# Kernel optimization log

Measured on AMD Instinct MI355X. Metric: run time of the kernel, lower is better.

Reference implementation:

```python
import jax, jax.numpy as jnp
import numpy as np
from jax import lax

MODES = 16
DEPTH = 8
NPH = 8  # photons = sum(init_state); init_state = [1]*8 + [0]*8
IDX = np.arange(NPH)  # output_indices derived from init_state
PI = np.pi
CHUNK = 4096  # pairs per permanent chunk (memory control, mirrors chunk_subsets idea)


def setup_inputs() -> dict:
    key = jax.random.key(0)
    k1, k2, k3 = jax.random.split(key, 3)
    x = jax.random.normal(k1, (256, 64), dtype=jnp.float32)
    W = jax.random.normal(k2, (120, 64), dtype=jnp.float32) / np.sqrt(64.0)
    b = jax.random.normal(k3, (120,), dtype=jnp.float32) * 0.01
    return {"x": x, "W": W, "b": b}


def _forward(x, W, b):
    N = x.shape[0]
    # fc1 + sigmoid embedding -> angle pairs
    x_emb = jax.nn.sigmoid(x @ W.T + b)              # (N, 120)
    tbu = x_emb.reshape(N, -1, 2)                    # (N, T, 2)
    theta = tbu[:, :, 0] * (PI / 2)
    phi = tbu[:, :, 1] * (2 * PI)
    ct = jnp.cos(theta).astype(jnp.complex64)
    st = jnp.sin(theta).astype(jnp.complex64)
    ep = jnp.exp(1j * phi.astype(jnp.complex64))
    # 2x2 tunable beam-splitter unitaries: [[e^{i phi} c, -s], [e^{i phi} s, c]]
    row0 = jnp.stack([ep * ct, -st], axis=-1)
    row1 = jnp.stack([ep * st, ct], axis=-1)
    blocks = jnp.stack([row0, row1], axis=-2)        # (N, T, 2, 2)

    # Apply block-diagonal layers. Block-diag matmul only mixes row pairs,
    # so update row segments directly instead of building (modes,modes) UBS.
    U = jnp.broadcast_to(jnp.eye(MODES, dtype=jnp.complex64), (N, MODES, MODES))
    nb_even, nb_odd = MODES // 2, (MODES - 2) // 2
    n_before = 0
    for d in range(DEPTH):
        if d % 2 == 0:
            nb, off = nb_even, 0
        else:
            nb, off = nb_odd, 1
        blk = blocks[:, n_before:n_before + nb]                      # (N, nb, 2, 2)
        seg = U[:, off:off + 2 * nb, :].reshape(N, nb, 2, MODES)     # row pairs
        new = jnp.einsum('nkab,nkbm->nkam', blk, seg).reshape(N, 2 * nb, MODES)
        U = U.at[:, off:off + 2 * nb, :].set(new)
        n_before += nb

    # Photonic Gram: K[a,b] = |perm( (U_a^dag U_b)[idx, idx] )|^2.
    # Only the idx-columns of U enter: V = U[:, :, idx], submatrix = V_a^dag V_b.
    V = U[:, :, IDX]                                  # (N, MODES, n)
    G = jnp.einsum('ami,bmj->abij', V.conj(), V)      # (N, N, n, n)

    n = NPH
    subsets = jnp.arange(1, 1 << n)                   # (S,), S = 2^n - 1
    masks = (subsets[:, None] >> jnp.arange(n)[None, :]) & 1   # (S, n)
    signs = (1 - 2 * ((n - masks.sum(axis=1)) & 1)).astype(jnp.complex64)
    maskc = masks.astype(jnp.complex64)

    A = G.reshape(N * N, n, n)
    nc = (N * N) // CHUNK

    def perm_chunk(Ac):  # Ryser: sum_S (-1)^{n-|S|} prod_i sum_{j in S} A_ij
        ss = jnp.einsum('cij,sj->csi', Ac, maskc)     # (c, S, n) subset row-sums
        pr = jnp.prod(ss, axis=2)                     # (c, S)
        return jnp.sum(pr * signs, axis=1)            # (c,)

    perms = lax.map(perm_chunk, A.reshape(nc, CHUNK, n, n)).reshape(N * N)
    K = (jnp.abs(perms) ** 2).astype(jnp.float32).reshape(N, N)
    di = jnp.arange(N)
    K = K.at[di, di].set(1.0)
    return x_emb, K


def reference(x, W, b):
    return _forward(x, W, b)
```

## Files before the change

### kernel.cpp

```cpp
#include <hip/hip_runtime.h>
#include <math.h>

#define NS 256
#define EMB 120
#define NBLK 60
#define MODES 16
#define NPH 8

typedef float v2f __attribute__((ext_vector_type(2)));

__device__ __forceinline__ v2f cmul(v2f a, v2f b) {
    v2f axx = {a.x, a.x};
    v2f nyy = {-a.y, a.y};
    v2f byx = {b.y, b.x};
    return axx * b + nyy * byx;
}
__device__ __forceinline__ v2f cfma_conj(v2f a, v2f b, v2f c) {
    v2f axx = {a.x, a.x};
    v2f pyy = {a.y, -a.y};
    v2f byx = {b.y, b.x};
    return axx * b + (pyy * byx + c);
}

__device__ __forceinline__ float dpp_xor1(float x) {
    return __builtin_bit_cast(float,
        __builtin_amdgcn_mov_dpp(__builtin_bit_cast(int, x), 0xB1, 0xF, 0xF, true));
}
__device__ __forceinline__ float dpp_xor2(float x) {
    return __builtin_bit_cast(float,
        __builtin_amdgcn_mov_dpp(__builtin_bit_cast(int, x), 0x4E, 0xF, 0xF, true));
}

__global__ __launch_bounds__(128) void emb_v_kernel(
    const float* __restrict__ x, const float* __restrict__ W,
    const float* __restrict__ bias, float* __restrict__ out_emb,
    float2* __restrict__ Vws)
{
    const int s = blockIdx.x;
    const int t = threadIdx.x;
    __shared__ float emb[EMB];
    __shared__ float ctA[NBLK], stA[NBLK], exA[NBLK], eyA[NBLK];

    if (t < EMB) {
        const float* xr = x + s * 64;
        const float* wr = W + t * 64;
        float acc = bias[t];
        #pragma unroll
        for (int k = 0; k < 64; ++k) acc = fmaf(xr[k], wr[k], acc);
        float e = 1.0f / (1.0f + expf(-acc));
        emb[t] = e;
        out_emb[s * EMB + t] = e;
    }
    __syncthreads();

    if (t < NBLK) {
        float th = emb[2 * t]     * 1.57079632679489662f;
        float ph = emb[2 * t + 1] * 6.28318530717958648f;
        float st, ct, sp, cp;
        sincosf(th, &st, &ct);
        sincosf(ph, &sp, &cp);
        ctA[t] = ct; stA[t] = st; exA[t] = cp; eyA[t] = sp;
    }
    __syncthreads();

    if (t < NPH) {
        const int c = t;
        float2 u[MODES];
        #pragma unroll
        for (int m = 0; m < MODES; ++m) {
            u[m].x = (m == c) ? 1.0f : 0.0f;
            u[m].y = 0.0f;
        }
        int bi = 0;
        #pragma unroll
        for (int d = 0; d < 8; ++d) {
            const int off = d & 1;
            const int nb = 8 - off;
            #pragma unroll
            for (int k = 0; k < nb; ++k) {
                float ct = ctA[bi], st = stA[bi], ex = exA[bi], ey = eyA[bi];
                ++bi;
                const int r0 = off + 2 * k;
                float2 u0 = u[r0], u1 = u[r0 + 1];
                float2 n0, n1;
                n0.x = ex * ct * u0.x - ey * ct * u0.y - st * u1.x;
                n0.y = ex * ct * u0.y + ey * ct * u0.x - st * u1.y;
                n1.x = ex * st * u0.x - ey * st * u0.y + ct * u1.x;
                n1.y = ex * st * u0.y + ey * st * u0.x + ct * u1.y;
                u[r0] = n0; u[r0 + 1] = n1;
            }
        }
        #pragma unroll
        for (int m = 0; m < MODES; ++m)
            Vws[(s * MODES + m) * NPH + c] = u[m];
    }
}

__global__ __launch_bounds__(256, 2) void perm_kernel(
    const float2* __restrict__ Vws, float* __restrict__ outK)
{
    __shared__ float2 sva[8][132];
    __shared__ float2 svb[8][132];

    const int L = blockIdx.x;
    int t = (int)((65.0f - sqrtf(4225.0f - 8.0f * (float)L)) * 0.5f);
    while (t * (65 - t) / 2 > L) --t;
    while ((t + 1) * (65 - (t + 1)) / 2 <= L) ++t;
    const int ta = t;
    const int tb = ta + (L - t * (65 - t) / 2);

    const int tid = threadIdx.x;
    const float4* srcA = (const float4*)(Vws + (size_t)ta * 8 * 128);
    const float4* srcB = (const float4*)(Vws + (size_t)tb * 8 * 128);
    #pragma unroll
    for (int r = 0; r < 2; ++r) {
        int idx = r * 256 + tid;
        int row = idx >> 6;
        int c4  = idx & 63;
        *(float4*)&sva[row][c4 * 2] = srcA[idx];
        *(float4*)&svb[row][c4 * 2] = srcB[idx];
    }
    __syncthreads();

    const int p   = tid >> 2;
    const int sub = tid & 3;
    const int h   = sub & 1;
    const int e   = sub >> 1;
    const int pa  = p >> 3;
    const int pb  = p & 7;

    v2f Go[2][8];
    #pragma unroll
    for (int i = 0; i < 2; ++i)
        #pragma unroll
        for (int j = 0; j < 8; ++j) Go[i][j] = (v2f){0.f, 0.f};

    #pragma unroll 2
    for (int m = 0; m < 16; ++m) {
        float4 va4 = *(const float4*)&sva[pa][m * 8 + 4 * h + 2 * e];
        v2f a0 = {va4.x, va4.y};
        v2f a1 = {va4.z, va4.w};
        v2f vb[8];
        #pragma unroll
        for (int jj = 0; jj < 4; ++jj) {
            float4 b4 = *(const float4*)&svb[pb][m * 8 + 2 * jj];
            vb[2 * jj]     = (v2f){b4.x, b4.y};
            vb[2 * jj + 1] = (v2f){b4.z, b4.w};
        }
        #pragma unroll
        for (int j = 0; j < 8; ++j) {
            Go[0][j] = cfma_conj(a0, vb[j], Go[0][j]);
            Go[1][j] = cfma_conj(a1, vb[j], Go[1][j]);
        }
    }

    v2f Gp[2][8];
    #pragma unroll
    for (int i = 0; i < 2; ++i)
        #pragma unroll
        for (int j = 0; j < 8; ++j) {
            Gp[i][j].x = dpp_xor2(Go[i][j].x);
            Gp[i][j].y = dpp_xor2(Go[i][j].y);
        }

    const float sgn = 1.0f - 2.0f * (float)e;
    const v2f sgnv = {sgn, sgn};
    v2f rs[4];
    #pragma unroll
    for (int r = 0; r < 2; ++r) {
        {
            v2f s = ((Go[r][0] + Go[r][1]) + (Go[r][2] + Go[r][3]))
                  + ((Go[r][4] + Go[r][5]) + Go[r][6]);
            rs[r] = sgnv * Go[r][7] + s;
        }
        {
            v2f s = ((Gp[r][0] + Gp[r][1]) + (Gp[r][2] + Gp[r][3]))
                  + ((Gp[r][4] + Gp[r][5]) + Gp[r][6]);
            rs[2 + r] = sgnv * Gp[r][7] + s;
        }
    }

    v2f acc;

#define TREE(OUT) do {                                                \
        v2f t01 = cmul(rs[0], rs[1]);                                 \
        v2f t23 = cmul(rs[2], rs[3]);                                 \
        v2f half = cmul(t01, t23);                                    \
        v2f oth;                                                      \
        oth.x = dpp_xor1(half.x);                                     \
        oth.y = dpp_xor1(half.y);                                     \
        OUT = cmul(half, oth);                                        \
    } while (0)

#define UPD(J, S) do {                                                \
        const v2f sv = {(S), (S)};                                    \
        rs[0] = sv * Go[0][J] + rs[0];                                \
        rs[1] = sv * Go[1][J] + rs[1];                                \
        rs[2] = sv * Gp[0][J] + rs[2];                                \
        rs[3] = sv * Gp[1][J] + rs[3];                                \
    } while (0)

#define TERM(TS) do {                                                 \
        v2f fullp; TREE(fullp);                                       \
        const v2f tv = {(TS), (TS)};                                  \
        acc = tv * fullp + acc;                                       \
    } while (0)

    TREE(acc);

    #pragma unroll 1
    for (int o = 0; o < 8; ++o) {
        const float s4 = (o & 1) ? 2.f : -2.f;
        UPD(1, -2.f); TERM(-1.f);
        UPD(2, -2.f); TERM( 1.f);
        UPD(1,  2.f); TERM(-1.f);
        UPD(3,  s4 ); TERM( 1.f);
        UPD(1, -2.f); TERM(-1.f);
        UPD(2,  2.f); TERM( 1.f);
        UPD(1,  2.f); TERM(-1.f);
        if (o < 7) {
            const int qq = o + 1;
            const int cz = __builtin_ctz(qq);
            const float s8 = ((qq >> (cz + 1)) & 1) ? 2.f : -2.f;
            const bool is4 = (cz == 0);
            const bool is5 = (cz == 1);
            const v2f s8v = {s8, s8};
            #pragma unroll
            for (int r = 0; r < 2; ++r) {
                v2f co = is4 ? Go[r][4] : (is5 ? Go[r][5] : Go[r][6]);
                v2f cp = is4 ? Gp[r][4] : (is5 ? Gp[r][5] : Gp[r][6]);
                rs[r]     = s8v * co + rs[r];
                rs[2 + r] = s8v * cp + rs[2 + r];
            }
            TERM(1.f);
        }
    }
#undef UPD
#undef TERM
#undef TREE

    float ax = sgn * acc.x, ay = sgn * acc.y;
    ax += dpp_xor2(ax);
    ay += dpp_xor2(ay);

    if (sub == 0) {
        const int a = ta * 8 + pa;
        const int b = tb * 8 + pb;
        float K = fmaf(ax, ax, ay * ay) * (1.0f / 16384.0f);
        if (a == b) K = 1.0f;
        outK[a * 256 + b] = K;
        outK[b * 256 + a] = K;
    }
}

extern "C" void kernel_launch(void* const* d_in, const int* in_sizes, int n_in,
                              void* d_out, int out_size, void* d_ws, size_t ws_size,
                              hipStream_t stream) {
    const float* x    = (const float*)d_in[0];
    const float* W    = (const float*)d_in[1];
    const float* bias = (const float*)d_in[2];
    float* out     = (float*)d_out;
    float* out_emb = out;
    float* outK    = out + NS * EMB;
    float2* Vws    = (float2*)d_ws;

    emb_v_kernel<<<NS, 128, 0, stream>>>(x, W, bias, out_emb, Vws);
    perm_kernel<<<528, 256, 0, stream>>>(Vws, outK);
}
```

Baseline: 80.14 us.

## Pair Gray-code subsets differing in column 6 and fully unroll Ryser loop

```diff
diff --git a/kernel.cpp b/kernel.cpp
--- a/kernel.cpp
+++ b/kernel.cpp
@@ -165,26 +165,29 @@
 
     const float sgn = 1.0f - 2.0f * (float)e;
     const v2f sgnv = {sgn, sgn};
-    v2f rs[4];
+    const v2f m2   = {-2.f, -2.f};
+    v2f rsa[4], rsb[4];
     #pragma unroll
     for (int r = 0; r < 2; ++r) {
         {
             v2f s = ((Go[r][0] + Go[r][1]) + (Go[r][2] + Go[r][3]))
                   + ((Go[r][4] + Go[r][5]) + Go[r][6]);
-            rs[r] = sgnv * Go[r][7] + s;
+            rsa[r] = sgnv * Go[r][7] + s;
+            rsb[r] = m2 * Go[r][6] + rsa[r];
         }
         {
             v2f s = ((Gp[r][0] + Gp[r][1]) + (Gp[r][2] + Gp[r][3]))
                   + ((Gp[r][4] + Gp[r][5]) + Gp[r][6]);
-            rs[2 + r] = sgnv * Gp[r][7] + s;
+            rsa[2 + r] = sgnv * Gp[r][7] + s;
+            rsb[2 + r] = m2 * Gp[r][6] + rsa[2 + r];
         }
     }
 
     v2f acc;
 
-#define TREE(OUT) do {                                                \
-        v2f t01 = cmul(rs[0], rs[1]);                                 \
-        v2f t23 = cmul(rs[2], rs[3]);                                 \
+#define TREEQ(RS, OUT) do {                                           \
+        v2f t01 = cmul((RS)[0], (RS)[1]);                             \
+        v2f t23 = cmul((RS)[2], (RS)[3]);                             \
         v2f half = cmul(t01, t23);                                    \
         v2f oth;                                                      \
         oth.x = dpp_xor1(half.x);                                     \
@@ -192,52 +195,68 @@
         OUT = cmul(half, oth);                                        \
     } while (0)
 
-#define UPD(J, S) do {                                                \
+#define UPD2(J, S) do {                                               \
         const v2f sv = {(S), (S)};                                    \
-        rs[0] = sv * Go[0][J] + rs[0];                                \
-        rs[1] = sv * Go[1][J] + rs[1];                                \
-        rs[2] = sv * Gp[0][J] + rs[2];                                \
-        rs[3] = sv * Gp[1][J] + rs[3];                                \
+        rsa[0] = sv * Go[0][J] + rsa[0];                              \
+        rsa[1] = sv * Go[1][J] + rsa[1];                              \
+        rsa[2] = sv * Gp[0][J] + rsa[2];                              \
+        rsa[3] = sv * Gp[1][J] + rsa[3];                              \
+        rsb[0] = sv * Go[0][J] + rsb[0];                              \
+        rsb[1] = sv * Go[1][J] + rsb[1];                              \
+        rsb[2] = sv * Gp[0][J] + rsb[2];                              \
+        rsb[3] = sv * Gp[1][J] + rsb[3];                              \
     } while (0)
 
-#define TERM(TS) do {                                                 \
-        v2f fullp; TREE(fullp);                                       \
+#define STEP(J, S, TS) do {                                           \
+        UPD2(J, S);                                                   \
+        v2f fa, fb;                                                   \
+        TREEQ(rsa, fa);                                               \
+        TREEQ(rsb, fb);                                               \
         const v2f tv = {(TS), (TS)};                                  \
-        acc = tv * fullp + acc;                                       \
+        acc = tv * fa + acc;                                          \
+        acc = (-tv) * fb + acc;                                       \
     } while (0)
 
-    TREE(acc);
-
-    #pragma unroll 1
-    for (int o = 0; o < 8; ++o) {
-        const float s4 = (o & 1) ? 2.f : -2.f;
-        UPD(1, -2.f); TERM(-1.f);
-        UPD(2, -2.f); TERM( 1.f);
-        UPD(1,  2.f); TERM(-1.f);
-        UPD(3,  s4 ); TERM( 1.f);
-        UPD(1, -2.f); TERM(-1.f);
-        UPD(2,  2.f); TERM( 1.f);
-        UPD(1,  2.f); TERM(-1.f);
-        if (o < 7) {
-            const int qq = o + 1;
-            const int cz = __builtin_ctz(qq);
-            const float s8 = ((qq >> (cz + 1)) & 1) ? 2.f : -2.f;
-            const bool is4 = (cz == 0);
-            const bool is5 = (cz == 1);
-            const v2f s8v = {s8, s8};
-            #pragma unroll
-            for (int r = 0; r < 2; ++r) {
-                v2f co = is4 ? Go[r][4] : (is5 ? Go[r][5] : Go[r][6]);
-                v2f cp = is4 ? Gp[r][4] : (is5 ? Gp[r][5] : Gp[r][6]);
-                rs[r]     = s8v * co + rs[r];
-                rs[2 + r] = s8v * cp + rs[2 + r];
-            }
-            TERM(1.f);
-        }
-    }
-#undef UPD
-#undef TERM
-#undef TREE
+    {
+        v2f fa, fb;
+        TREEQ(rsa, fa);
+        TREEQ(rsb, fb);
+        acc = fa - fb;
+    }
+    STEP(1, -2.f, -1.f);
+    STEP(2, -2.f,  1.f);
+    STEP(1,  2.f, -1.f);
+    STEP(3, -2.f,  1.f);
+    STEP(1, -2.f, -1.f);
+    STEP(2,  2.f,  1.f);
+    STEP(1,  2.f, -1.f);
+    STEP(4, -2.f,  1.f);
+    STEP(1, -2.f, -1.f);
+    STEP(2, -2.f,  1.f);
+    STEP(1,  2.f, -1.f);
+    STEP(3,  2.f,  1.f);
+    STEP(1, -2.f, -1.f);
+    STEP(2,  2.f,  1.f);
+    STEP(1,  2.f, -1.f);
+    STEP(5, -2.f,  1.f);
+    STEP(1, -2.f, -1.f);
+    STEP(2, -2.f,  1.f);
+    STEP(1,  2.f, -1.f);
+    STEP(3, -2.f,  1.f);
+    STEP(1, -2.f, -1.f);
+    STEP(2,  2.f,  1.f);
+    STEP(1,  2.f, -1.f);
+    STEP(4,  2.f,  1.f);
+    STEP(1, -2.f, -1.f);
+    STEP(2, -2.f,  1.f);
+    STEP(1,  2.f, -1.f);
+    STEP(3,  2.f,  1.f);
+    STEP(1, -2.f, -1.f);
+    STEP(2,  2.f,  1.f);
+    STEP(1,  2.f, -1.f);
+#undef STEP
+#undef UPD2
+#undef TREEQ
 
     float ax = sgn * acc.x, ay = sgn * acc.y;
     ax += dpp_xor2(ax);
```

Result: faster. 76.57 us (-4.4%).
